# Performance work log

Measured on AMD Instinct MI355X. Metric: run time of the kernel, lower is better.

The kernel has to match this reference:

```python
import jax, jax.numpy as jnp
import numpy as np

B, H, W = 64, 448, 448
OUT = 256          # kornia resize target
PAD = 20           # torch.randint(20, ...) padding range
HB, WB = H + 2 * (PAD - 1), W + 2 * (PAD - 1)  # bg large enough for any padded crop


def setup_inputs():
    key = jax.random.key(0)
    k = jax.random.split(key, 10)
    img = jax.random.uniform(k[0], (B, 3, H, W), jnp.float32)
    # wc: zero background, random nonzero rectangle per sample (document region)
    y0 = jax.random.randint(k[1], (B,), 10, 80)
    y1 = jax.random.randint(k[2], (B,), H - 80, H - 10)
    x0 = jax.random.randint(k[3], (B,), 10, 80)
    x1 = jax.random.randint(k[4], (B,), W - 80, W - 10)
    ys = jnp.arange(H)[None, :, None]
    xs = jnp.arange(W)[None, None, :]
    rect = ((ys >= y0[:, None, None]) & (ys <= y1[:, None, None]) &
            (xs >= x0[:, None, None]) & (xs <= x1[:, None, None]))
    vals = jax.random.uniform(k[5], (B, 3, H, W), jnp.float32, 0.1, 1.0)
    wc = jnp.where(rect[:, None, :, :], vals, 0.0)
    bm = jax.random.uniform(k[6], (B, 2, H, W), jnp.float32) * W
    bg = jax.random.uniform(k[7], (B, 3, HB, WB), jnp.float32)
    rand_color = jax.random.uniform(k[8], (B, 3), jnp.float32)
    kj = jax.random.split(k[9], 5)
    brightness = jax.random.uniform(kj[0], (B,), jnp.float32, 0.9, 1.1)
    contrast = jax.random.uniform(kj[1], (B,), jnp.float32, 0.9, 1.1)
    saturation = jax.random.uniform(kj[2], (B,), jnp.float32, 0.9, 1.1)
    hue = jax.random.uniform(kj[3], (B,), jnp.float32, -0.1, 0.1)
    c = jax.random.randint(kj[4], (B, 5), 0, PAD, jnp.int32)
    return dict(img=img, wc=wc, bm=bm, bg=bg, rand_color=rand_color,
                brightness=brightness, contrast=contrast,
                saturation=saturation, hue=hue, c=c)


def rgb_to_hsv(x, eps=1e-8):
    r, g, b = x[:, 0], x[:, 1], x[:, 2]
    mx = jnp.max(x, axis=1)
    mn = jnp.min(x, axis=1)
    d = mx - mn
    hr = ((g - b) / (d + eps)) % 6.0
    hg = (b - r) / (d + eps) + 2.0
    hb = (r - g) / (d + eps) + 4.0
    h = jnp.where(mx == r, hr, jnp.where(mx == g, hg, hb)) / 6.0
    h = jnp.where(d <= eps, 0.0, h)
    s = d / (mx + eps)
    return h, s, mx


def hsv_to_rgb(h, s, v):
    h6 = (h % 1.0) * 6.0
    i = jnp.floor(h6)
    f = h6 - i
    p = v * (1.0 - s)
    q = v * (1.0 - f * s)
    t = v * (1.0 - (1.0 - f) * s)
    i = i.astype(jnp.int32) % 6
    conds = [i == 0, i == 1, i == 2, i == 3, i == 4, i == 5]
    r = jnp.select(conds, [v, q, p, p, t, v])
    g = jnp.select(conds, [t, v, v, q, p, p])
    b = jnp.select(conds, [p, p, t, v, v, q])
    return jnp.stack([r, g, b], axis=1)


def _per_sample(img1, m1, bg1, bm1, c1, col1):
    # nonzero bounding box of mask (equivalent to nonzero + min/max)
    row_any = jnp.any(m1, axis=1)
    col_any = jnp.any(m1, axis=0)
    miny = jnp.argmax(row_any)
    maxy = H - 1 - jnp.argmax(row_any[::-1])
    minx = jnp.argmax(col_any)
    maxx = W - 1 - jnp.argmax(col_any[::-1])
    Hp = maxy - miny + 1 + c1[2] + c1[3]   # padded crop height
    Wp = maxx - minx + 1 + c1[0] + c1[1]   # padded crop width

    # bilinear resize (align_corners=False) source coords in padded frame
    def src_coords(size):
        s = (jnp.arange(OUT, dtype=jnp.float32) + 0.5) * (size.astype(jnp.float32) / OUT) - 0.5
        s = jnp.maximum(s, 0.0)
        i0 = jnp.floor(s).astype(jnp.int32)
        w = s - i0
        i0 = jnp.minimum(i0, size - 1)
        i1 = jnp.minimum(i0 + 1, size - 1)
        return i0, i1, w
    y0, y1, wy = src_coords(Hp)
    x0, x1, wx = src_coords(Wp)

    # composited (crop+pad+mask+background) image evaluated at padded-frame pixels
    def comp_at(py, px):
        oy = py - c1[2] + miny
        ox = px - c1[0] + minx
        valid = (oy >= miny) & (oy <= maxy) & (ox >= minx) & (ox <= maxx)
        oyc = jnp.clip(oy, 0, H - 1)
        oxc = jnp.clip(ox, 0, W - 1)
        mval = jnp.where(valid, m1[oyc, oxc], False).astype(jnp.float32)  # [256,256]
        ival = img1[:, oyc, oxc] * mval                                   # [3,256,256]
        bgv = bg1[:, jnp.clip(py, 0, HB - 1), jnp.clip(px, 0, WB - 1)]
        bgpix = jnp.where(c1[4] > 2, bgv, col1[:, None, None])
        return ival + bgpix * (1.0 - mval)

    c00 = comp_at(y0[:, None], x0[None, :])
    c01 = comp_at(y0[:, None], x1[None, :])
    c10 = comp_at(y1[:, None], x0[None, :])
    c11 = comp_at(y1[:, None], x1[None, :])
    top = c00 * (1.0 - wx) + c01 * wx
    bot = c10 * (1.0 - wx) + c11 * wx
    out = top * (1.0 - wy)[None, :, None] + bot * wy[None, :, None]

    bm_x = (bm1[0] - minx.astype(jnp.float32) + c1[0]) / Wp * 2.0 - 1.0
    bm_y = (bm1[1] - miny.astype(jnp.float32) + c1[2]) / Hp * 2.0 - 1.0
    return out, jnp.stack([bm_x, bm_y])


def _forward(img, wc, bm, bg, rand_color, brightness, contrast, saturation, hue, c):
    mask = (wc[:, 0] != 0) & (wc[:, 1] != 0) & (wc[:, 2] != 0)
    out, bm_out = jax.vmap(_per_sample)(img, mask, bg, bm, c, rand_color)
    # ColorJitter(0.1,0.1,0.1,0.1), fixed order: brightness, contrast, saturation, hue
    def gray(u):
        return 0.299 * u[:, 0] + 0.587 * u[:, 1] + 0.114 * u[:, 2]
    x = jnp.clip(out * brightness[:, None, None, None], 0.0, 1.0)
    cf = contrast[:, None, None, None]
    mean = gray(x).mean(axis=(1, 2))[:, None, None, None]
    x = jnp.clip(cf * x + (1.0 - cf) * mean, 0.0, 1.0)
    sf = saturation[:, None, None, None]
    x = jnp.clip(sf * x + (1.0 - sf) * gray(x)[:, None], 0.0, 1.0)
    h, s, v = rgb_to_hsv(x)
    h = (h + hue[:, None, None]) % 1.0
    x = jnp.clip(hsv_to_rgb(h, s, v), 0.0, 1.0)
    return x, bm_out


def reference(img, wc, bm, bg, rand_color, brightness, contrast, saturation, hue, c):
    return _forward(img, wc, bm, bg, rand_color, brightness, contrast, saturation, hue, c)
```

## Files before the change

### kernel.cpp

```cpp
#include <hip/hip_runtime.h>
#include <hip/hip_fp16.h>

#define B_    64
#define H_    448
#define W_    448
#define OUT_  256
#define HB_   486
#define WB_   486
#define HW_   (H_*W_)
#define OO_   (OUT_*OUT_)
#define F4PP  (HW_/4)
#define F4PB  (F4PP/16)
#define MBPS  (HW_/8)
#define BMF4S (2*HW_/4)
#define BM4PB (BMF4S/256)

typedef float fx4 __attribute__((ext_vector_type(4)));
typedef unsigned long long u64;

__device__ __forceinline__ float clip01(float v) { return fminf(fmaxf(v, 0.f), 1.f); }
__device__ __forceinline__ float pmodf_(float a, float m) {
  float r = fmodf(a, m);
  return (r < 0.f) ? r + m : r;
}

struct Params {
  int minx, miny, maxx, maxy, c0, c2, usebg, Hp, Wp;
  float scX, scY, offx, szx, offy, szy;
};

__device__ __forceinline__ Params make_params(const int* __restrict__ pb,
                                              const int* __restrict__ cbuf, int s) {
  int mnX = W_, mxX = -1, mnY = H_, mxY = -1;
  #pragma unroll
  for (int t = 0; t < 16; ++t) {
    int base = (s*16 + t) * 4;
    mnX = min(mnX, pb[base+0]); mxX = max(mxX, pb[base+1]);
    mnY = min(mnY, pb[base+2]); mxY = max(mxY, pb[base+3]);
  }
  if (mxY < 0) { mnY = 0; mxY = H_-1; }
  if (mxX < 0) { mnX = 0; mxX = W_-1; }
  int c0 = cbuf[s*5+0], c1 = cbuf[s*5+1], c2 = cbuf[s*5+2],
      c3 = cbuf[s*5+3], c4 = cbuf[s*5+4];
  Params P;
  P.minx = mnX; P.miny = mnY; P.maxx = mxX; P.maxy = mxY;
  P.c0 = c0; P.c2 = c2; P.usebg = (c4 > 2);
  P.Hp = mxY - mnY + 1 + c2 + c3;
  P.Wp = mxX - mnX + 1 + c0 + c1;
  P.scX = (float)P.Wp / (float)OUT_;
  P.scY = (float)P.Hp / (float)OUT_;
  P.offx = (float)(mnX - c0); P.szx = (float)P.Wp;
  P.offy = (float)(mnY - c2); P.szy = (float)P.Hp;
  return P;
}

__global__ void k1_bboxmask(const float* __restrict__ wc, unsigned char* __restrict__ maskbits,
                            int* __restrict__ pb, int useMask) {
  int blk = blockIdx.x, tid = threadIdx.x;
  int s = blk >> 4, slot = blk & 15;
  const fx4* w0 = (const fx4*)(wc + (size_t)s*3*HW_);
  const fx4* w1 = w0 + F4PP;
  const fx4* w2 = w1 + F4PP;
  unsigned char* mbs = maskbits + (size_t)s*MBPS;
  int lane = tid & 63;
  int mnX = W_, mxX = -1, mnY = H_, mxY = -1;
  for (int j = tid; j < F4PB; j += 256) {
    int i = slot*F4PB + j;
    fx4 a = __builtin_nontemporal_load(w0 + i);
    fx4 b = __builtin_nontemporal_load(w1 + i);
    fx4 c = __builtin_nontemporal_load(w2 + i);
    int m0 = (a.x != 0.f && b.x != 0.f && c.x != 0.f);
    int m1 = (a.y != 0.f && b.y != 0.f && c.y != 0.f);
    int m2 = (a.z != 0.f && b.z != 0.f && c.z != 0.f);
    int m3 = (a.w != 0.f && b.w != 0.f && c.w != 0.f);
    if (useMask) {
      int nib = m0 | (m1<<1) | (m2<<2) | (m3<<3);
      int nxt = __shfl(nib, lane + 1, 64);
      if ((lane & 1) == 0)
        mbs[i >> 1] = (unsigned char)(nib | (nxt << 4));
    }
    if (m0 | m1 | m2 | m3) {
      int y  = i / 112;
      int x0 = (i - y*112) * 4;
      mnY = min(mnY, y); mxY = max(mxY, y);
      int first = m0 ? 0 : (m1 ? 1 : (m2 ? 2 : 3));
      int last  = m3 ? 3 : (m2 ? 2 : (m1 ? 1 : 0));
      mnX = min(mnX, x0 + first);
      mxX = max(mxX, x0 + last);
    }
  }
  __shared__ int sr[4][256];
  sr[0][tid]=mnX; sr[1][tid]=mxX; sr[2][tid]=mnY; sr[3][tid]=mxY;
  __syncthreads();
  for (int off = 128; off > 0; off >>= 1) {
    if (tid < off) {
      sr[0][tid] = min(sr[0][tid], sr[0][tid+off]);
      sr[1][tid] = max(sr[1][tid], sr[1][tid+off]);
      sr[2][tid] = min(sr[2][tid], sr[2][tid+off]);
      sr[3][tid] = max(sr[3][tid], sr[3][tid+off]);
    }
    __syncthreads();
  }
  if (tid == 0) {
    pb[blk*4+0] = sr[0][0]; pb[blk*4+1] = sr[1][0];
    pb[blk*4+2] = sr[2][0]; pb[blk*4+3] = sr[3][0];
  }
}

__global__ void k2_compose(const float* __restrict__ img, const float* __restrict__ bg,
                           const float* __restrict__ wc, const unsigned char* __restrict__ maskbits,
                           const float* __restrict__ col, const float* __restrict__ bri,
                           const int* __restrict__ pb, const int* __restrict__ cbuf,
                           const float* __restrict__ bm, float* __restrict__ bmout,
                           __half* __restrict__ xh, float* __restrict__ xout,
                           float* __restrict__ gpart, int useMask, int useHalf) {
  int tid = threadIdx.x;
  int pphys = blockIdx.x;
  int blk = (pphys & 7) * 2048 + (pphys >> 3);
  int s = blk >> 8;
  int slot = blk & 255;
  int p = (slot << 8) | tid;
  int py = slot, px = tid;

  const fx4* bm4 = (const fx4*)(bm + (size_t)s*2*HW_);
  int j0 = slot*BM4PB + tid;
  int j1 = j0 + 256;
  bool h1 = (tid + 256) < BM4PB;
  fx4 bv0 = __builtin_nontemporal_load(bm4 + j0);
  fx4 bv1 = h1 ? __builtin_nontemporal_load(bm4 + j1) : (fx4){0.f,0.f,0.f,0.f};

  Params P = make_params(pb, cbuf, s);
  float colr = col[s*3+0], colg = col[s*3+1], colb = col[s*3+2];
  float brf = bri[s];

  float sy = fmaxf((py + 0.5f) * P.scY - 0.5f, 0.f);
  int   y0 = (int)sy;
  float wy = sy - (float)y0;
  y0 = min(y0, P.Hp - 1);
  int y1 = min(y0 + 1, P.Hp - 1);

  float sx = fmaxf((px + 0.5f) * P.scX - 0.5f, 0.f);
  int   x0 = (int)sx;
  float wx = sx - (float)x0;
  x0 = min(x0, P.Wp - 1);
  int x1 = min(x0 + 1, P.Wp - 1);

  const float* imgb = img + (size_t)s*3*HW_;
  const float* bgb  = bg  + (size_t)s*3*HB_*WB_;
  const float* w0p  = wc  + (size_t)s*3*HW_;
  const unsigned char* mbs = maskbits + (size_t)s*MBPS;

  int oy0 = y0 - P.c2 + P.miny, oy1 = y1 - P.c2 + P.miny;
  int ox0 = x0 - P.c0 + P.minx, ox1 = x1 - P.c0 + P.minx;
  bool vy0 = (oy0 >= P.miny) && (oy0 <= P.maxy);
  bool vy1 = (oy1 >= P.miny) && (oy1 <= P.maxy);
  bool vx0 = (ox0 >= P.minx) && (ox0 <= P.maxx);
  bool vx1 = (ox1 >= P.minx) && (ox1 <= P.maxx);
  int oy0c = min(max(oy0, 0), H_-1), oy1c = min(max(oy1, 0), H_-1);
  int ox0c = min(max(ox0, 0), W_-1), ox1c = min(max(ox1, 0), W_-1);
  int by0 = min(y0, HB_-1), by1 = min(y1, HB_-1);
  int bx0 = min(x0, WB_-1), bx1 = min(x1, WB_-1);

  int mi00 = oy0c*W_ + ox0c, mi01 = oy0c*W_ + ox1c;
  int mi10 = oy1c*W_ + ox0c, mi11 = oy1c*W_ + ox1c;

  float m00, m01, m10, m11;
  if (useMask) {
    m00 = (float)((mbs[mi00 >> 3] >> (mi00 & 7)) & 1);
    m01 = (float)((mbs[mi01 >> 3] >> (mi01 & 7)) & 1);
    m10 = (float)((mbs[mi10 >> 3] >> (mi10 & 7)) & 1);
    m11 = (float)((mbs[mi11 >> 3] >> (mi11 & 7)) & 1);
  } else {
    m00 = (w0p[mi00] != 0.f && w0p[mi00+HW_] != 0.f && w0p[mi00+2*HW_] != 0.f) ? 1.f : 0.f;
    m01 = (w0p[mi01] != 0.f && w0p[mi01+HW_] != 0.f && w0p[mi01+2*HW_] != 0.f) ? 1.f : 0.f;
    m10 = (w0p[mi10] != 0.f && w0p[mi10+HW_] != 0.f && w0p[mi10+2*HW_] != 0.f) ? 1.f : 0.f;
    m11 = (w0p[mi11] != 0.f && w0p[mi11+HW_] != 0.f && w0p[mi11+2*HW_] != 0.f) ? 1.f : 0.f;
  }
  if (!(vy0 && vx0)) m00 = 0.f;
  if (!(vy0 && vx1)) m01 = 0.f;
  if (!(vy1 && vx0)) m10 = 0.f;
  if (!(vy1 && vx1)) m11 = 0.f;

  bool needImg = __any(m00 + m01 + m10 + m11 > 0.f);
  bool needBg  = __any(m00 * m01 * m10 * m11 < 1.f);

  float i00[3] = {0.f,0.f,0.f}, i01[3] = {0.f,0.f,0.f};
  float i10[3] = {0.f,0.f,0.f}, i11[3] = {0.f,0.f,0.f};
  if (needImg) {
    #pragma unroll
    for (int ch = 0; ch < 3; ++ch) {
      size_t o = (size_t)ch*HW_;
      i00[ch] = imgb[o + mi00]; i01[ch] = imgb[o + mi01];
      i10[ch] = imgb[o + mi10]; i11[ch] = imgb[o + mi11];
    }
  }

  float g00[3], g01[3], g10[3], g11[3];
  if (P.usebg) {
    if (needBg) {
      size_t b00 = (size_t)by0*WB_ + bx0, b01 = (size_t)by0*WB_ + bx1;
      size_t b10 = (size_t)by1*WB_ + bx0, b11 = (size_t)by1*WB_ + bx1;
      const size_t PL = (size_t)HB_*WB_;
      #pragma unroll
      for (int ch = 0; ch < 3; ++ch) {
        g00[ch] = bgb[b00 + ch*PL];
        g01[ch] = bgb[b01 + ch*PL];
        g10[ch] = bgb[b10 + ch*PL];
        g11[ch] = bgb[b11 + ch*PL];
      }
    } else {
      #pragma unroll
      for (int ch = 0; ch < 3; ++ch) { g00[ch]=g01[ch]=g10[ch]=g11[ch]=0.f; }
    }
  } else {
    g00[0]=g01[0]=g10[0]=g11[0]=colr;
    g00[1]=g01[1]=g10[1]=g11[1]=colg;
    g00[2]=g01[2]=g10[2]=g11[2]=colb;
  }

  float xr[3];
  float gsum;
  {
    #pragma unroll
    for (int ch = 0; ch < 3; ++ch) {
      float a00 = i00[ch]*m00 + g00[ch]*(1.f-m00);
      float a01 = i01[ch]*m01 + g01[ch]*(1.f-m01);
      float a10 = i10[ch]*m10 + g10[ch]*(1.f-m10);
      float a11 = i11[ch]*m11 + g11[ch]*(1.f-m11);
      float top = a00*(1.f-wx) + a01*wx;
      float bot = a10*(1.f-wx) + a11*wx;
      float o = top*(1.f-wy) + bot*wy;
      xr[ch] = clip01(o * brf);
      size_t oi = (size_t)(s*3 + ch)*OO_ + p;
      if (useHalf) {
        __half hv = __float2half(xr[ch]);
        __builtin_nontemporal_store(*(const unsigned short*)&hv,
                                    (unsigned short*)(xh + oi));
      } else {
        xout[oi] = xr[ch];
      }
    }
    gsum = 0.299f*xr[0] + 0.587f*xr[1] + 0.114f*xr[2];
  }

  #pragma unroll
  for (int off = 32; off > 0; off >>= 1)
    gsum += __shfl_xor(gsum, off, 64);
  __shared__ float swv[4];
  int wv = tid >> 6, lane = tid & 63;
  if (lane == 0) swv[wv] = gsum;
  __syncthreads();
  if (tid == 0) gpart[blk] = swv[0] + swv[1] + swv[2] + swv[3];

  {
    fx4* out4 = (fx4*)(bmout + (size_t)s*2*HW_);
    float invx = 2.f / P.szx, invy = 2.f / P.szy;
    {
      float off_ = (j0 < F4PP) ? P.offx : P.offy;
      float inv  = (j0 < F4PP) ? invx  : invy;
      fx4 o;
      o.x = (bv0.x - off_) * inv - 1.f;
      o.y = (bv0.y - off_) * inv - 1.f;
      o.z = (bv0.z - off_) * inv - 1.f;
      o.w = (bv0.w - off_) * inv - 1.f;
      __builtin_nontemporal_store(o, out4 + j0);
    }
    if (h1) {
      float off_ = (j1 < F4PP) ? P.offx : P.offy;
      float inv  = (j1 < F4PP) ? invx  : invy;
      fx4 o;
      o.x = (bv1.x - off_) * inv - 1.f;
      o.y = (bv1.y - off_) * inv - 1.f;
      o.z = (bv1.z - off_) * inv - 1.f;
      o.w = (bv1.w - off_) * inv - 1.f;
      __builtin_nontemporal_store(o, out4 + j1);
    }
  }
}

__global__ void kb_color(const __half* __restrict__ xh, const float* __restrict__ gpart,
                         const float* __restrict__ con, const float* __restrict__ sat,
                         const float* __restrict__ hue, float* __restrict__ xout,
                         int useHalf) {
  int tid = threadIdx.x, blk = blockIdx.x;
  int s = blk >> 6, slot = blk & 63;
  int u = slot*256 + tid;

  float sum = 0.f;
  for (int t = 0; t < 256; ++t) sum += gpart[s*256 + t];
  float mean = sum * (1.f / (float)OO_);
  float cf = con[s], sfc = sat[s], hu = hue[s];

  float in[3][4];
  #pragma unroll
  for (int ch = 0; ch < 3; ++ch) {
    size_t base = (size_t)(s*3 + ch)*OO_ + (size_t)u*4;
    if (useHalf) {
      u64 q = __builtin_nontemporal_load((const u64*)(xh + base));
      unsigned q0 = (unsigned)q, q1 = (unsigned)(q >> 32);
      __half2 h01 = *(__half2*)&q0;
      __half2 h23 = *(__half2*)&q1;
      float2 f01 = __half22float2(h01);
      float2 f23 = __half22float2(h23);
      in[ch][0]=f01.x; in[ch][1]=f01.y; in[ch][2]=f23.x; in[ch][3]=f23.y;
    } else {
      float4 f = ((const float4*)xout)[base >> 2];
      in[ch][0]=f.x; in[ch][1]=f.y; in[ch][2]=f.z; in[ch][3]=f.w;
    }
  }

  float ro[4], go[4], bo[4];
  #pragma unroll
  for (int l = 0; l < 4; ++l) {
    float r = in[0][l], g = in[1][l], bl = in[2][l];
    r  = clip01(cf*r  + (1.f-cf)*mean);
    g  = clip01(cf*g  + (1.f-cf)*mean);
    bl = clip01(cf*bl + (1.f-cf)*mean);

    float gr = 0.299f*r + 0.587f*g + 0.114f*bl;
    r  = clip01(sfc*r  + (1.f-sfc)*gr);
    g  = clip01(sfc*g  + (1.f-sfc)*gr);
    bl = clip01(sfc*bl + (1.f-sfc)*gr);

    const float eps = 1e-8f;
    float mx = fmaxf(r, fmaxf(g, bl));
    float mn = fminf(r, fminf(g, bl));
    float d  = mx - mn;
    float inv = 1.f / (d + eps);
    float h;
    if (mx == r)      h = pmodf_((g - bl) * inv, 6.f);
    else if (mx == g) h = (bl - r) * inv + 2.f;
    else              h = (r - g) * inv + 4.f;
    h *= (1.f/6.f);
    if (d <= eps) h = 0.f;
    float sv = d / (mx + eps);
    float v  = mx;

    h = pmodf_(h + hu, 1.f);

    float h6 = pmodf_(h, 1.f) * 6.f;
    float fi = floorf(h6);
    float f  = h6 - fi;
    int   i6 = ((int)fi) % 6;
    float pp = v * (1.f - sv);
    float q  = v * (1.f - f*sv);
    float t  = v * (1.f - (1.f - f)*sv);
    float rr, gg, bb;
    switch (i6) {
      case 0:  rr=v;  gg=t;  bb=pp; break;
      case 1:  rr=q;  gg=v;  bb=pp; break;
      case 2:  rr=pp; gg=v;  bb=t;  break;
      case 3:  rr=pp; gg=q;  bb=v;  break;
      case 4:  rr=t;  gg=pp; bb=v;  break;
      default: rr=v;  gg=pp; bb=q;  break;
    }
    ro[l] = clip01(rr); go[l] = clip01(gg); bo[l] = clip01(bb);
  }
  size_t ub = (size_t)(s*3)*OO_ + (size_t)u*4;
  fx4 vr = {ro[0],ro[1],ro[2],ro[3]};
  fx4 vg = {go[0],go[1],go[2],go[3]};
  fx4 vb = {bo[0],bo[1],bo[2],bo[3]};
  __builtin_nontemporal_store(vr, (fx4*)xout + ((ub)                 >> 2));
  __builtin_nontemporal_store(vg, (fx4*)xout + ((ub +   (size_t)OO_) >> 2));
  __builtin_nontemporal_store(vb, (fx4*)xout + ((ub + 2*(size_t)OO_) >> 2));
}

extern "C" void kernel_launch(void* const* d_in, const int* in_sizes, int n_in,
                              void* d_out, int out_size, void* d_ws, size_t ws_size,
                              hipStream_t stream) {
  const float* img = (const float*)d_in[0];
  const float* wc  = (const float*)d_in[1];
  const float* bm  = (const float*)d_in[2];
  const float* bg  = (const float*)d_in[3];
  const float* col = (const float*)d_in[4];
  const float* bri = (const float*)d_in[5];
  const float* con = (const float*)d_in[6];
  const float* sat = (const float*)d_in[7];
  const float* hue = (const float*)d_in[8];
  const int*   cb  = (const int*)d_in[9];

  float* outx  = (float*)d_out;
  float* outbm = outx + (size_t)B_*3*OO_;

  char* ws = (char*)d_ws;
  int*   pb    = (int*)ws;
  float* gpart = (float*)(ws + 16384);
  unsigned char* maskbits = (unsigned char*)(ws + 81920);
  __half* xh = (__half*)(ws + 1687552);

  size_t needMask = 81920 + (size_t)B_*MBPS;
  size_t needHalf = 1687552 + (size_t)B_*3*OO_*2;
  int useMask = (ws_size >= needMask) ? 1 : 0;
  int useHalf = (ws_size >= needHalf) ? 1 : 0;

  k1_bboxmask<<<1024,  256, 0, stream>>>(wc, maskbits, pb, useMask);
  k2_compose <<<16384, 256, 0, stream>>>(img, bg, wc, maskbits, col, bri, pb, cb,
                                         bm, outbm, xh, outx, gpart,
                                         useMask, useHalf);
  kb_color   <<<4096,  256, 0, stream>>>(xh, gpart, con, sat, hue, outx, useHalf);
}
```

Baseline: 125.4 us.

## Skip loading wc channels 1-2 in zero regions and precompute per-sample params

In the bbox/mask kernel, channels 1 and 2 of wc are now loaded only when some lane in the wavefront has a nonzero channel-0 value, which cuts memory traffic over the zero background. A new single-block kernel reduces the per-block bbox partials and crop parameters into a per-sample table once. The compose kernel then reads that table instead of every thread redoing the 16-way reduction. The cost is an extra tiny kernel launch and a divergent load path.

```diff
diff --git a/kernel.cpp b/kernel.cpp
--- a/kernel.cpp
+++ b/kernel.cpp
@@ -27,32 +27,8 @@
 struct Params {
   int minx, miny, maxx, maxy, c0, c2, usebg, Hp, Wp;
   float scX, scY, offx, szx, offy, szy;
+  int pad;
 };
-
-__device__ __forceinline__ Params make_params(const int* __restrict__ pb,
-                                              const int* __restrict__ cbuf, int s) {
-  int mnX = W_, mxX = -1, mnY = H_, mxY = -1;
-  #pragma unroll
-  for (int t = 0; t < 16; ++t) {
-    int base = (s*16 + t) * 4;
-    mnX = min(mnX, pb[base+0]); mxX = max(mxX, pb[base+1]);
-    mnY = min(mnY, pb[base+2]); mxY = max(mxY, pb[base+3]);
-  }
-  if (mxY < 0) { mnY = 0; mxY = H_-1; }
-  if (mxX < 0) { mnX = 0; mxX = W_-1; }
-  int c0 = cbuf[s*5+0], c1 = cbuf[s*5+1], c2 = cbuf[s*5+2],
-      c3 = cbuf[s*5+3], c4 = cbuf[s*5+4];
-  Params P;
-  P.minx = mnX; P.miny = mnY; P.maxx = mxX; P.maxy = mxY;
-  P.c0 = c0; P.c2 = c2; P.usebg = (c4 > 2);
-  P.Hp = mxY - mnY + 1 + c2 + c3;
-  P.Wp = mxX - mnX + 1 + c0 + c1;
-  P.scX = (float)P.Wp / (float)OUT_;
-  P.scY = (float)P.Hp / (float)OUT_;
-  P.offx = (float)(mnX - c0); P.szx = (float)P.Wp;
-  P.offy = (float)(mnY - c2); P.szy = (float)P.Hp;
-  return P;
-}
 
 __global__ void k1_bboxmask(const float* __restrict__ wc, unsigned char* __restrict__ maskbits,
                             int* __restrict__ pb, int useMask) {
@@ -67,12 +43,16 @@
   for (int j = tid; j < F4PB; j += 256) {
     int i = slot*F4PB + j;
     fx4 a = __builtin_nontemporal_load(w0 + i);
-    fx4 b = __builtin_nontemporal_load(w1 + i);
-    fx4 c = __builtin_nontemporal_load(w2 + i);
-    int m0 = (a.x != 0.f && b.x != 0.f && c.x != 0.f);
-    int m1 = (a.y != 0.f && b.y != 0.f && c.y != 0.f);
-    int m2 = (a.z != 0.f && b.z != 0.f && c.z != 0.f);
-    int m3 = (a.w != 0.f && b.w != 0.f && c.w != 0.f);
+    bool nz0 = (a.x != 0.f) || (a.y != 0.f) || (a.z != 0.f) || (a.w != 0.f);
+    int m0 = 0, m1 = 0, m2 = 0, m3 = 0;
+    if (__any(nz0)) {
+      fx4 b = __builtin_nontemporal_load(w1 + i);
+      fx4 c = __builtin_nontemporal_load(w2 + i);
+      m0 = (a.x != 0.f && b.x != 0.f && c.x != 0.f);
+      m1 = (a.y != 0.f && b.y != 0.f && c.y != 0.f);
+      m2 = (a.z != 0.f && b.z != 0.f && c.z != 0.f);
+      m3 = (a.w != 0.f && b.w != 0.f && c.w != 0.f);
+    }
     if (useMask) {
       int nib = m0 | (m1<<1) | (m2<<2) | (m3<<3);
       int nxt = __shfl(nib, lane + 1, 64);
@@ -107,10 +87,38 @@
   }
 }
 
+__global__ void k0_params(const int* __restrict__ pb, const int* __restrict__ cbuf,
+                          Params* __restrict__ ptab) {
+  int b = threadIdx.x;
+  if (b >= B_) return;
+  int mnX = W_, mxX = -1, mnY = H_, mxY = -1;
+  #pragma unroll
+  for (int t = 0; t < 16; ++t) {
+    int base = (b*16 + t) * 4;
+    mnX = min(mnX, pb[base+0]); mxX = max(mxX, pb[base+1]);
+    mnY = min(mnY, pb[base+2]); mxY = max(mxY, pb[base+3]);
+  }
+  if (mxY < 0) { mnY = 0; mxY = H_-1; }
+  if (mxX < 0) { mnX = 0; mxX = W_-1; }
+  int c0 = cbuf[b*5+0], c1 = cbuf[b*5+1], c2 = cbuf[b*5+2],
+      c3 = cbuf[b*5+3], c4 = cbuf[b*5+4];
+  Params P;
+  P.minx = mnX; P.miny = mnY; P.maxx = mxX; P.maxy = mxY;
+  P.c0 = c0; P.c2 = c2; P.usebg = (c4 > 2);
+  P.Hp = mxY - mnY + 1 + c2 + c3;
+  P.Wp = mxX - mnX + 1 + c0 + c1;
+  P.scX = (float)P.Wp / (float)OUT_;
+  P.scY = (float)P.Hp / (float)OUT_;
+  P.offx = (float)(mnX - c0); P.szx = (float)P.Wp;
+  P.offy = (float)(mnY - c2); P.szy = (float)P.Hp;
+  P.pad = 0;
+  ptab[b] = P;
+}
+
 __global__ void k2_compose(const float* __restrict__ img, const float* __restrict__ bg,
                            const float* __restrict__ wc, const unsigned char* __restrict__ maskbits,
                            const float* __restrict__ col, const float* __restrict__ bri,
-                           const int* __restrict__ pb, const int* __restrict__ cbuf,
+                           const Params* __restrict__ ptab,
                            const float* __restrict__ bm, float* __restrict__ bmout,
                            __half* __restrict__ xh, float* __restrict__ xout,
                            float* __restrict__ gpart, int useMask, int useHalf) {
@@ -129,7 +137,7 @@
   fx4 bv0 = __builtin_nontemporal_load(bm4 + j0);
   fx4 bv1 = h1 ? __builtin_nontemporal_load(bm4 + j1) : (fx4){0.f,0.f,0.f,0.f};
 
-  Params P = make_params(pb, cbuf, s);
+  Params P = ptab[s];
   float colr = col[s*3+0], colg = col[s*3+1], colb = col[s*3+2];
   float brf = bri[s];
 
@@ -383,18 +391,20 @@
   float* outbm = outx + (size_t)B_*3*OO_;
 
   char* ws = (char*)d_ws;
-  int*   pb    = (int*)ws;
-  float* gpart = (float*)(ws + 16384);
-  unsigned char* maskbits = (unsigned char*)(ws + 81920);
-  __half* xh = (__half*)(ws + 1687552);
-
-  size_t needMask = 81920 + (size_t)B_*MBPS;
-  size_t needHalf = 1687552 + (size_t)B_*3*OO_*2;
+  int*    pb    = (int*)ws;
+  float*  gpart = (float*)(ws + 16384);
+  Params* ptab  = (Params*)(ws + 81920);
+  unsigned char* maskbits = (unsigned char*)(ws + 86016);
+  __half* xh = (__half*)(ws + 1691648);
+
+  size_t needMask = 86016 + (size_t)B_*MBPS;
+  size_t needHalf = 1691648 + (size_t)B_*3*OO_*2;
   int useMask = (ws_size >= needMask) ? 1 : 0;
   int useHalf = (ws_size >= needHalf) ? 1 : 0;
 
   k1_bboxmask<<<1024,  256, 0, stream>>>(wc, maskbits, pb, useMask);
-  k2_compose <<<16384, 256, 0, stream>>>(img, bg, wc, maskbits, col, bri, pb, cb,
+  k0_params  <<<1,     64,  0, stream>>>(pb, cb, ptab);
+  k2_compose <<<16384, 256, 0, stream>>>(img, bg, wc, maskbits, col, bri, ptab,
                                          bm, outbm, xh, outx, gpart,
                                          useMask, useHalf);
   kb_color   <<<4096,  256, 0, stream>>>(xh, gpart, con, sat, hue, outx, useHalf);
```

Measured after the change: 125.0 us. Within noise of the previous version (-0.3%).
